# Kernel tuning notes

Measured on AMD Instinct MI355X. Metric: run time of the kernel, lower is better.

## Reference

```python
import jax, jax.numpy as jnp
import numpy as np
import math

EPS = 1e-6


def setup_inputs() -> dict:
    key = jax.random.key(0)
    k1, k2 = jax.random.split(key)
    B, S, D, F = 4, 4096, 2048, 2048
    x = jax.random.normal(k1, (B, S, D), dtype=jnp.float32)
    weight = jax.random.normal(k2, (F, D), dtype=jnp.float32) / np.sqrt(D)
    alpha = jnp.ones((1,), dtype=jnp.float32)
    bias = jnp.zeros((F,), dtype=jnp.float32)
    return {"x": x, "weight": weight, "alpha": alpha, "bias": bias}


def reference(x, weight, alpha, bias):
    F = weight.shape[0]
    # y: [B, S, F]
    y = jnp.einsum("bsd,fd->bsf", x, weight)
    x_sq = jnp.sum(x * x, axis=-1, keepdims=True)        # [B, S, 1]
    w_sq = jnp.sum(weight * weight, axis=-1)              # [F]
    distances = x_sq + w_sq - 2.0 * y                     # squared Euclidean dist
    out = (y * y) / (distances + EPS)
    scale = (math.sqrt(F) / math.log(1.0 + F)) ** alpha   # alpha shape (1,) broadcasts
    out = out * scale + bias
    return out
```

## Files before the change

### kernel.cpp

```cpp
#include <hip/hip_runtime.h>
#include <hip/hip_bf16.h>
#include <cstdint>
#include <cstddef>


typedef __bf16 bf16_t;
typedef __bf16 bf16x8 __attribute__((ext_vector_type(8)));
typedef __bf16 bf16x4 __attribute__((ext_vector_type(4)));
typedef float f32x4 __attribute__((ext_vector_type(4)));

constexpr int M_DIM = 16384;
constexpr int N_DIM = 2048;
constexpr int K_DIM = 2048;
constexpr int BM = 256, BN = 256, BK = 64;
constexpr int KT = K_DIM / BK;
constexpr int SEG = 128 * 64;

__device__ __forceinline__ void async16(const bf16_t* g, bf16_t* l) {
    __builtin_amdgcn_global_load_lds(
        (const __attribute__((address_space(1))) void*)g,
        (__attribute__((address_space(3))) void*)l,
        16, 0, 0);
}

__global__ __launch_bounds__(256) void prep_convert(const float* __restrict__ x,
                                                    const float* __restrict__ w,
                                                    bf16_t* __restrict__ xb,
                                                    bf16_t* __restrict__ wb,
                                                    float* __restrict__ xsq,
                                                    float* __restrict__ wsq) {
    const int row = blockIdx.x;
    const float* src;
    bf16_t* dstb;
    float* dsts;
    if (row < M_DIM) {
        src = x + (size_t)row * K_DIM;
        dstb = xb + (size_t)row * K_DIM;
        dsts = xsq + row;
    } else {
        const int r = row - M_DIM;
        src = w + (size_t)r * K_DIM;
        dstb = wb + (size_t)r * K_DIM;
        dsts = wsq + r;
    }
    const float4* s4 = (const float4*)src;
    const float4 a = s4[threadIdx.x];
    const float4 b = s4[threadIdx.x + 256];
    float s = a.x * a.x + a.y * a.y + a.z * a.z + a.w * a.w
            + b.x * b.x + b.y * b.y + b.z * b.z + b.w * b.w;
    bf16x4 av = { (bf16_t)a.x, (bf16_t)a.y, (bf16_t)a.z, (bf16_t)a.w };
    bf16x4 bv = { (bf16_t)b.x, (bf16_t)b.y, (bf16_t)b.z, (bf16_t)b.w };
    ((bf16x4*)dstb)[threadIdx.x] = av;
    ((bf16x4*)dstb)[threadIdx.x + 256] = bv;
#pragma unroll
    for (int off = 32; off > 0; off >>= 1) s += __shfl_down(s, off, 64);
    __shared__ float red[4];
    const int lane = threadIdx.x & 63;
    const int wv = threadIdx.x >> 6;
    if (lane == 0) red[wv] = s;
    __syncthreads();
    if (threadIdx.x == 0) *dsts = red[0] + red[1] + red[2] + red[3];
}

__global__ __launch_bounds__(512, 2) void yat_gemm(const bf16_t* __restrict__ A,
                                                   const bf16_t* __restrict__ Bw,
                                                   const float* __restrict__ xsq,
                                                   const float* __restrict__ wsq,
                                                   const float* __restrict__ bias,
                                                   const float* __restrict__ alpha,
                                                   float* __restrict__ out) {
    __shared__ bf16_t sA[4 * SEG];
    __shared__ bf16_t sB[4 * SEG];

    const int tid = (int)threadIdx.x;
    const int lane = tid & 63;
    const int wv = tid >> 6;
    const int wm = wv >> 2;
    const int wn = wv & 3;

    const int bm = (int)blockIdx.x >> 3;
    const int bn = (int)blockIdx.x & 7;

    const int frm = lane & 15;
    const int jch = lane >> 4;
    const int sx = frm & 7;

    const int st_r = tid >> 3;
    const int st_g = (tid & 7) ^ (st_r & 7);
    const bf16_t* Ast = A + (size_t)(bm * BM + st_r) * K_DIM + st_g * 8;
    const bf16_t* Bst = Bw + (size_t)(bn * BN + st_r) * K_DIM + st_g * 8;

    auto stageA = [&](int kt, int h) {
        if (kt >= KT) return;
        bf16_t* d = sA + ((kt * 2 + h) & 3) * SEG + tid * 8;
        const bf16_t* s = Ast + (size_t)(h * 128) * K_DIM + kt * 64;
        async16(s, d);
        async16(s + (size_t)64 * K_DIM, d + 4096);
    };
    auto stageB = [&](int kt, int h) {
        if (kt >= KT) return;
        bf16_t* d = sB + ((kt * 2 + h) & 3) * SEG + tid * 8;
        const bf16_t* s = Bst + (size_t)(h * 128) * K_DIM + kt * 64;
        async16(s, d);
        async16(s + (size_t)64 * K_DIM, d + 4096);
    };

    f32x4 acc[8][4] = {};
    bf16x8 bfr[4][2];

    stageB(0, 0); stageB(0, 1);
    stageA(0, 0); stageA(0, 1);
    stageB(1, 0); stageB(1, 1);
    asm volatile("s_waitcnt vmcnt(4)" ::: "memory");
    asm volatile("s_barrier" ::: "memory");

#define PHASE(Q, KTT, SMAT, SKT, SH, VMEND)                                     \
    {                                                                           \
        if ((Q) == 0) {                                                         \
            const int bslot = (((KTT) * 2 + (wn >> 1)) & 3) * SEG;              \
            _Pragma("unroll") for (int j = 0; j < 4; ++j) {                     \
                const int brow = (wn & 1) * 64 + j * 16 + frm;                  \
                _Pragma("unroll") for (int kk = 0; kk < 2; ++kk)                \
                    bfr[j][kk] = *(const bf16x8*)&sB[bslot + brow * 64 +        \
                                                    (((kk * 4 + jch) ^ sx) * 8)]; \
            }                                                                   \
        }                                                                       \
        bf16x8 af[2][2];                                                        \
        {                                                                       \
            const int aslot = (((KTT) * 2 + wm) & 3) * SEG;                     \
            _Pragma("unroll") for (int i2 = 0; i2 < 2; ++i2) {                  \
                const int arow = ((Q) * 2 + i2) * 16 + frm;                     \
                _Pragma("unroll") for (int kk = 0; kk < 2; ++kk)                \
                    af[i2][kk] = *(const bf16x8*)&sA[aslot + arow * 64 +        \
                                                    (((kk * 4 + jch) ^ sx) * 8)]; \
            }                                                                   \
        }                                                                       \
        if ((SMAT) == 0) stageA((SKT), (SH)); else stageB((SKT), (SH));         \
        asm volatile("s_barrier" ::: "memory");                                 \
        __builtin_amdgcn_s_setprio(1);                                          \
        _Pragma("unroll") for (int kk = 0; kk < 2; ++kk)                        \
            _Pragma("unroll") for (int i2 = 0; i2 < 2; ++i2)                    \
                _Pragma("unroll") for (int j = 0; j < 4; ++j)                   \
                    acc[(Q) * 2 + i2][j] = __builtin_amdgcn_mfma_f32_16x16x32_bf16( \
                        af[i2][kk], bfr[j][kk], acc[(Q) * 2 + i2][j], 0, 0, 0); \
        __builtin_amdgcn_s_setprio(0);                                          \
        if (VMEND) {                                                            \
            if ((SKT) >= KT) { asm volatile("s_waitcnt vmcnt(0)" ::: "memory"); } \
            else             { asm volatile("s_waitcnt vmcnt(4)" ::: "memory"); } \
        }                                                                       \
        asm volatile("s_barrier" ::: "memory");                                 \
    }

#pragma unroll 1
    for (int u = 0; u < KT / 2; ++u) {
        const int a = 2 * u, b = 2 * u + 1;
        PHASE(0, a, 0, b,     0, 0)
        PHASE(1, a, 0, b,     1, 0)
        PHASE(2, a, 1, a + 2, 0, 0)
        PHASE(3, a, 1, a + 2, 1, 1)
        PHASE(0, b, 0, a + 2, 0, 0)
        PHASE(1, b, 0, a + 2, 1, 0)
        PHASE(2, b, 1, b + 2, 0, 0)
        PHASE(3, b, 1, b + 2, 1, 1)
    }
#undef PHASE

    const float sc = powf(sqrtf((float)N_DIM) / logf(1.0f + (float)N_DIM), alpha[0]);
    float wsq_c[4], bias_c[4];
#pragma unroll
    for (int j = 0; j < 4; ++j) {
        const int col = bn * BN + wn * 64 + j * 16 + frm;
        wsq_c[j] = wsq[col];
        bias_c[j] = bias[col];
    }
#pragma unroll
    for (int i = 0; i < 8; ++i) {
#pragma unroll
        for (int r = 0; r < 4; ++r) {
            const int row = bm * BM + wm * 128 + i * 16 + jch * 4 + r;
            const float xs = xsq[row];
            float* orow = out + (size_t)row * N_DIM + bn * BN + wn * 64 + frm;
#pragma unroll
            for (int j = 0; j < 4; ++j) {
                const float y = acc[i][j][r];
                const float d = xs + wsq_c[j] - 2.0f * y + 1e-6f;
                orow[j * 16] = (y * y) / d * sc + bias_c[j];
            }
        }
    }
}

extern "C" void kernel_launch(void* const* d_in, const int* in_sizes, int n_in,
                              void* d_out, int out_size, void* d_ws, size_t ws_size,
                              hipStream_t stream) {
    (void)in_sizes; (void)n_in; (void)out_size; (void)ws_size;
    const float* x = (const float*)d_in[0];
    const float* w = (const float*)d_in[1];
    const float* alpha = (const float*)d_in[2];
    const float* bias = (const float*)d_in[3];
    float* out = (float*)d_out;

    bf16_t* xb = (bf16_t*)d_ws;
    bf16_t* wb = xb + (size_t)M_DIM * K_DIM;
    float* xsq = (float*)(wb + (size_t)N_DIM * K_DIM);
    float* wsq = xsq + M_DIM;

    prep_convert<<<M_DIM + N_DIM, 256, 0, stream>>>(x, w, xb, wb, xsq, wsq);
    yat_gemm<<<(M_DIM / BM) * (N_DIM / BN), 512, 0, stream>>>(xb, wb, xsq, wsq, bias, alpha, out);
}
```

Baseline: 359.5 us.

## Software-pipeline LDS fragment reads with double-buffered registers and rework prep kernel

The GEMM main loop now reads the next A/B fragments from LDS into alternate register buffers while the current MFMA batch runs, with sched_barrier fences and a reordered global-to-LDS staging and waitcnt schedule. This is meant to hide LDS read latency behind matrix math and drop one barrier per phase. The prep kernel now has each wave convert two full rows without shared-memory reduction, launching 8x fewer blocks. The extra register buffers raise VGPR pressure, and the hand-tuned waitcnt counts must match the new staging order.

```diff
diff --git a/kernel.cpp b/kernel.cpp
--- a/kernel.cpp
+++ b/kernel.cpp
@@ -29,37 +29,39 @@
                                                     bf16_t* __restrict__ wb,
                                                     float* __restrict__ xsq,
                                                     float* __restrict__ wsq) {
-    const int row = blockIdx.x;
-    const float* src;
-    bf16_t* dstb;
-    float* dsts;
-    if (row < M_DIM) {
-        src = x + (size_t)row * K_DIM;
-        dstb = xb + (size_t)row * K_DIM;
-        dsts = xsq + row;
-    } else {
-        const int r = row - M_DIM;
-        src = w + (size_t)r * K_DIM;
-        dstb = wb + (size_t)r * K_DIM;
-        dsts = wsq + r;
-    }
-    const float4* s4 = (const float4*)src;
-    const float4 a = s4[threadIdx.x];
-    const float4 b = s4[threadIdx.x + 256];
-    float s = a.x * a.x + a.y * a.y + a.z * a.z + a.w * a.w
-            + b.x * b.x + b.y * b.y + b.z * b.z + b.w * b.w;
-    bf16x4 av = { (bf16_t)a.x, (bf16_t)a.y, (bf16_t)a.z, (bf16_t)a.w };
-    bf16x4 bv = { (bf16_t)b.x, (bf16_t)b.y, (bf16_t)b.z, (bf16_t)b.w };
-    ((bf16x4*)dstb)[threadIdx.x] = av;
-    ((bf16x4*)dstb)[threadIdx.x + 256] = bv;
-#pragma unroll
-    for (int off = 32; off > 0; off >>= 1) s += __shfl_down(s, off, 64);
-    __shared__ float red[4];
     const int lane = threadIdx.x & 63;
     const int wv = threadIdx.x >> 6;
-    if (lane == 0) red[wv] = s;
-    __syncthreads();
-    if (threadIdx.x == 0) *dsts = red[0] + red[1] + red[2] + red[3];
+    const int base = blockIdx.x * 8 + wv * 2;
+#pragma unroll
+    for (int it = 0; it < 2; ++it) {
+        const int row = base + it;
+        const float* src;
+        bf16_t* dstb;
+        float* dsts;
+        if (row < M_DIM) {
+            src = x + (size_t)row * K_DIM;
+            dstb = xb + (size_t)row * K_DIM;
+            dsts = xsq + row;
+        } else {
+            const int r = row - M_DIM;
+            src = w + (size_t)r * K_DIM;
+            dstb = wb + (size_t)r * K_DIM;
+            dsts = wsq + r;
+        }
+        const float4* s4 = (const float4*)src;
+        bf16x4* d4 = (bf16x4*)dstb;
+        float s = 0.0f;
+#pragma unroll
+        for (int j = 0; j < 8; ++j) {
+            const float4 a = s4[lane + j * 64];
+            s += a.x * a.x + a.y * a.y + a.z * a.z + a.w * a.w;
+            bf16x4 v = { (bf16_t)a.x, (bf16_t)a.y, (bf16_t)a.z, (bf16_t)a.w };
+            d4[lane + j * 64] = v;
+        }
+#pragma unroll
+        for (int off = 32; off > 0; off >>= 1) s += __shfl_down(s, off, 64);
+        if (lane == 0) *dsts = s;
+    }
 }
 
 __global__ __launch_bounds__(512, 2) void yat_gemm(const bf16_t* __restrict__ A,
@@ -90,14 +92,17 @@
     const bf16_t* Ast = A + (size_t)(bm * BM + st_r) * K_DIM + st_g * 8;
     const bf16_t* Bst = Bw + (size_t)(bn * BN + st_r) * K_DIM + st_g * 8;
 
-    auto stageA = [&](int kt, int h) {
+    auto stageA2 = [&](int kt) {
         if (kt >= KT) return;
-        bf16_t* d = sA + ((kt * 2 + h) & 3) * SEG + tid * 8;
-        const bf16_t* s = Ast + (size_t)(h * 128) * K_DIM + kt * 64;
-        async16(s, d);
-        async16(s + (size_t)64 * K_DIM, d + 4096);
+#pragma unroll
+        for (int h = 0; h < 2; ++h) {
+            bf16_t* d = sA + ((kt * 2 + h) & 3) * SEG + tid * 8;
+            const bf16_t* s = Ast + (size_t)(h * 128) * K_DIM + kt * 64;
+            async16(s, d);
+            async16(s + (size_t)64 * K_DIM, d + 4096);
+        }
     };
-    auto stageB = [&](int kt, int h) {
+    auto stageB1 = [&](int kt, int h) {
         if (kt >= KT) return;
         bf16_t* d = sB + ((kt * 2 + h) & 3) * SEG + tid * 8;
         const bf16_t* s = Bst + (size_t)(h * 128) * K_DIM + kt * 64;
@@ -106,64 +111,106 @@
     };
 
     f32x4 acc[8][4] = {};
-    bf16x8 bfr[4][2];
-
-    stageB(0, 0); stageB(0, 1);
-    stageA(0, 0); stageA(0, 1);
-    stageB(1, 0); stageB(1, 1);
-    asm volatile("s_waitcnt vmcnt(4)" ::: "memory");
-    asm volatile("s_barrier" ::: "memory");
-
-#define PHASE(Q, KTT, SMAT, SKT, SH, VMEND)                                     \
-    {                                                                           \
-        if ((Q) == 0) {                                                         \
-            const int bslot = (((KTT) * 2 + (wn >> 1)) & 3) * SEG;              \
-            _Pragma("unroll") for (int j = 0; j < 4; ++j) {                     \
-                const int brow = (wn & 1) * 64 + j * 16 + frm;                  \
-                _Pragma("unroll") for (int kk = 0; kk < 2; ++kk)                \
-                    bfr[j][kk] = *(const bf16x8*)&sB[bslot + brow * 64 +        \
-                                                    (((kk * 4 + jch) ^ sx) * 8)]; \
-            }                                                                   \
-        }                                                                       \
-        bf16x8 af[2][2];                                                        \
-        {                                                                       \
-            const int aslot = (((KTT) * 2 + wm) & 3) * SEG;                     \
-            _Pragma("unroll") for (int i2 = 0; i2 < 2; ++i2) {                  \
-                const int arow = ((Q) * 2 + i2) * 16 + frm;                     \
-                _Pragma("unroll") for (int kk = 0; kk < 2; ++kk)                \
-                    af[i2][kk] = *(const bf16x8*)&sA[aslot + arow * 64 +        \
-                                                    (((kk * 4 + jch) ^ sx) * 8)]; \
-            }                                                                   \
-        }                                                                       \
-        if ((SMAT) == 0) stageA((SKT), (SH)); else stageB((SKT), (SH));         \
-        asm volatile("s_barrier" ::: "memory");                                 \
-        __builtin_amdgcn_s_setprio(1);                                          \
-        _Pragma("unroll") for (int kk = 0; kk < 2; ++kk)                        \
-            _Pragma("unroll") for (int i2 = 0; i2 < 2; ++i2)                    \
-                _Pragma("unroll") for (int j = 0; j < 4; ++j)                   \
-                    acc[(Q) * 2 + i2][j] = __builtin_amdgcn_mfma_f32_16x16x32_bf16( \
-                        af[i2][kk], bfr[j][kk], acc[(Q) * 2 + i2][j], 0, 0, 0); \
-        __builtin_amdgcn_s_setprio(0);                                          \
-        if (VMEND) {                                                            \
-            if ((SKT) >= KT) { asm volatile("s_waitcnt vmcnt(0)" ::: "memory"); } \
-            else             { asm volatile("s_waitcnt vmcnt(4)" ::: "memory"); } \
-        }                                                                       \
-        asm volatile("s_barrier" ::: "memory");                                 \
-    }
+    bf16x8 afA[2][2], afB[2][2];
+    bf16x8 bfrA[4][2], bfrB[4][2];
+
+#define AF_READ(DST, KTN, QN)                                                  \
+    {                                                                          \
+        const int aslot_ = (((KTN) * 2 + wm) & 3) * SEG;                       \
+        _Pragma("unroll") for (int i2 = 0; i2 < 2; ++i2)                       \
+            _Pragma("unroll") for (int kk = 0; kk < 2; ++kk)                   \
+                DST[i2][kk] = *(const bf16x8*)&sA[aslot_ +                     \
+                    (((QN) * 2 + i2) * 16 + frm) * 64 + (((kk * 4 + jch) ^ sx) * 8)]; \
+    }
+#define BF_READ(DST, BJ0, KTB)                                                 \
+    {                                                                          \
+        const int bslot_ = (((KTB) * 2 + (wn >> 1)) & 3) * SEG;                \
+        _Pragma("unroll") for (int jj = 0; jj < 2; ++jj)                       \
+            _Pragma("unroll") for (int kk = 0; kk < 2; ++kk)                   \
+                DST[(BJ0) + jj][kk] = *(const bf16x8*)&sB[bslot_ +             \
+                    ((wn & 1) * 64 + ((BJ0) + jj) * 16 + frm) * 64 +           \
+                    (((kk * 4 + jch) ^ sx) * 8)];                              \
+    }
+#define MFMA16(QC, AFC, BFC)                                                   \
+    __builtin_amdgcn_s_setprio(1);                                             \
+    _Pragma("unroll") for (int kk = 0; kk < 2; ++kk)                           \
+        _Pragma("unroll") for (int i2 = 0; i2 < 2; ++i2)                       \
+            _Pragma("unroll") for (int j = 0; j < 4; ++j)                      \
+                acc[(QC) * 2 + i2][j] = __builtin_amdgcn_mfma_f32_16x16x32_bf16( \
+                    AFC[i2][kk], BFC[j][kk], acc[(QC) * 2 + i2][j], 0, 0, 0);  \
+    __builtin_amdgcn_s_setprio(0);
+#define SCHED0 __builtin_amdgcn_sched_barrier(0);
+#define SBAR asm volatile("s_barrier" ::: "memory");
+#define VMC4 asm volatile("s_waitcnt vmcnt(4)" ::: "memory");
+#define VMC(SKT)                                                               \
+    if ((SKT) < KT) { VMC4 } else { asm volatile("s_waitcnt vmcnt(0)" ::: "memory"); }
+
+    stageA2(0);
+    stageB1(0, 0); stageB1(0, 1);
+    stageB1(1, 0); stageB1(1, 1);
+    VMC4
+    SBAR
+    AF_READ(afA, 0, 0)
+    BF_READ(bfrA, 0, 0)
+    BF_READ(bfrA, 2, 0)
 
 #pragma unroll 1
     for (int u = 0; u < KT / 2; ++u) {
-        const int a = 2 * u, b = 2 * u + 1;
-        PHASE(0, a, 0, b,     0, 0)
-        PHASE(1, a, 0, b,     1, 0)
-        PHASE(2, a, 1, a + 2, 0, 0)
-        PHASE(3, a, 1, a + 2, 1, 1)
-        PHASE(0, b, 0, a + 2, 0, 0)
-        PHASE(1, b, 0, a + 2, 1, 0)
-        PHASE(2, b, 1, b + 2, 0, 0)
-        PHASE(3, b, 1, b + 2, 1, 1)
-    }
-#undef PHASE
+        const int a = 2 * u, b = a + 1;
+        AF_READ(afB, a, 1)
+        stageA2(b);
+        SCHED0
+        MFMA16(0, afA, bfrA)
+        VMC4
+        SBAR
+        AF_READ(afA, a, 2)
+        BF_READ(bfrB, 0, b)
+        stageB1(a + 2, 0);
+        SCHED0
+        MFMA16(1, afB, bfrA)
+        SBAR
+        AF_READ(afB, a, 3)
+        BF_READ(bfrB, 2, b)
+        stageB1(a + 2, 1);
+        SCHED0
+        MFMA16(2, afA, bfrA)
+        VMC(a + 2)
+        SBAR
+        AF_READ(afA, b, 0)
+        SCHED0
+        MFMA16(3, afB, bfrA)
+        SBAR
+        AF_READ(afB, b, 1)
+        stageA2(a + 2);
+        SCHED0
+        MFMA16(0, afA, bfrB)
+        VMC(a + 2)
+        SBAR
+        AF_READ(afA, b, 2)
+        BF_READ(bfrA, 0, a + 2)
+        stageB1(b + 2, 0);
+        SCHED0
+        MFMA16(1, afB, bfrB)
+        SBAR
+        AF_READ(afB, b, 3)
+        BF_READ(bfrA, 2, a + 2)
+        stageB1(b + 2, 1);
+        SCHED0
+        MFMA16(2, afA, bfrB)
+        VMC(b + 2)
+        SBAR
+        AF_READ(afA, a + 2, 0)
+        SCHED0
+        MFMA16(3, afB, bfrB)
+        SBAR
+    }
+#undef AF_READ
+#undef BF_READ
+#undef MFMA16
+#undef SCHED0
+#undef SBAR
+#undef VMC4
+#undef VMC
 
     const float sc = powf(sqrtf((float)N_DIM) / logf(1.0f + (float)N_DIM), alpha[0]);
     float wsq_c[4], bias_c[4];
@@ -205,6 +252,6 @@
     float* xsq = (float*)(wb + (size_t)N_DIM * K_DIM);
     float* wsq = xsq + M_DIM;
 
-    prep_convert<<<M_DIM + N_DIM, 256, 0, stream>>>(x, w, xb, wb, xsq, wsq);
+    prep_convert<<<(M_DIM + N_DIM) / 8, 256, 0, stream>>>(x, w, xb, wb, xsq, wsq);
     yat_gemm<<<(M_DIM / BM) * (N_DIM / BN), 512, 0, stream>>>(xb, wb, xsq, wsq, bias, alpha, out);
 }
```

Measured after the change: 363.7 us. Within noise of the previous version (+1.2%).
